# Optimization experiments

Hardware: AMD Instinct MI355X
Metric: run time of the kernel (lower is better)

Reference implementation:

```python
import jax, jax.numpy as jnp
import numpy as np

D = 1024   # embed_dim
L = 8      # num_blocks
H = 8      # num_heads
T = 2048   # temporal length
DH = D // H


def _ln(x, g, b, eps):
    m = jnp.mean(x, axis=-1, keepdims=True)
    v = jnp.var(x, axis=-1, keepdims=True)
    return (x - m) * jax.lax.rsqrt(v + eps) * g + b


def setup_inputs() -> dict:
    key = jax.random.key(0)
    ks = iter(jax.random.split(key, 48))
    s = 0.02
    rn = lambda shape: jax.random.normal(next(ks), shape, jnp.float32) * s
    return {
        "video_features": jax.random.normal(next(ks), (1, T, 1024), jnp.float32),
        "audio_features": jax.random.normal(next(ks), (1, T, 128), jnp.float32),
        "ap_W1": rn((128, D // 2)), "ap_b1": jnp.zeros((D // 2,)),
        "ap_W2": rn((D // 2, D)), "ap_b2": jnp.zeros((D,)),
        "vp_W1": rn((1024, D // 2)), "vp_b1": jnp.zeros((D // 2,)),
        "vp_W2": rn((D // 2, D)), "vp_b2": jnp.zeros((D,)),
        "pre_ln_g": jnp.ones((D,)), "pre_ln_b": jnp.zeros((D,)),
        "blk_Wq": rn((L, D, D)), "blk_bq": jnp.zeros((L, D)),
        "blk_Wk": rn((L, D, D)), "blk_bk": jnp.zeros((L, D)),
        "blk_Wv": rn((L, D, D)), "blk_bv": jnp.zeros((L, D)),
        "blk_Wo": rn((L, D, D)), "blk_bo": jnp.zeros((L, D)),
        "blk_bias_k": rn((L, D)), "blk_bias_v": rn((L, D)),
        "blk_ln1_g": jnp.ones((L, D)), "blk_ln1_b": jnp.zeros((L, D)),
        "blk_ln2_g": jnp.ones((L, D)), "blk_ln2_b": jnp.zeros((L, D)),
        "blk_mW1": rn((L, D, 4 * D)), "blk_mb1": jnp.zeros((L, 4 * D)),
        "blk_mW2": rn((L, 4 * D, D)), "blk_mb2": jnp.zeros((L, D)),
        "lh_W1": rn((D, D // 2)), "lh_b1": jnp.zeros((D // 2,)),
        "lh_W2": rn((D // 2, 1)), "lh_b2": jnp.zeros((1,)),
        "threshold": jnp.float32(0.5),
    }


def reference(video_features, audio_features,
              ap_W1, ap_b1, ap_W2, ap_b2,
              vp_W1, vp_b1, vp_W2, vp_b2,
              pre_ln_g, pre_ln_b,
              blk_Wq, blk_bq, blk_Wk, blk_bk, blk_Wv, blk_bv, blk_Wo, blk_bo,
              blk_bias_k, blk_bias_v,
              blk_ln1_g, blk_ln1_b, blk_ln2_g, blk_ln2_b,
              blk_mW1, blk_mb1, blk_mW2, blk_mb2,
              lh_W1, lh_b1, lh_W2, lh_b2, threshold):
    # projectors (Linear -> ReLU -> Linear)
    a = jax.nn.relu(audio_features @ ap_W1 + ap_b1) @ ap_W2 + ap_b2   # [1,T,D]
    v = jax.nn.relu(video_features @ vp_W1 + vp_b1) @ vp_W2 + vp_b2   # [1,T,D]

    x = _ln(a, pre_ln_g, pre_ln_b, 1e-6)  # pre_transformer_layer LayerNorm

    def block(x, p):
        Wq, bq, Wk, bk, Wv, bv, Wo, bo, bkx, bvx, g1, b1, g2, b2, mW1, mb1, mW2, mb2 = p
        h = _ln(x, g1, b1, 1e-5)
        q = (h @ Wq + bq).reshape(1, T, H, DH)
        # cross K/V from projected video, plus the learned bias_k/bias_v token (add_bias_kv)
        k = jnp.concatenate([v @ Wk + bk, bkx[None, None, :]], axis=1).reshape(1, T + 1, H, DH)
        val = jnp.concatenate([v @ Wv + bv, bvx[None, None, :]], axis=1).reshape(1, T + 1, H, DH)
        scores = jnp.einsum('bthd,bshd->bhts', q, k) * (DH ** -0.5)   # [1,H,T,T+1]
        attn = jax.nn.softmax(scores, axis=-1)
        o = jnp.einsum('bhts,bshd->bthd', attn, val).reshape(1, T, D)
        x = x + o @ Wo + bo
        h2 = _ln(x, g2, b2, 1e-5)
        x = x + jax.nn.gelu(h2 @ mW1 + mb1) @ mW2 + mb2
        return x, None

    ps = (blk_Wq, blk_bq, blk_Wk, blk_bk, blk_Wv, blk_bv, blk_Wo, blk_bo,
          blk_bias_k, blk_bias_v, blk_ln1_g, blk_ln1_b, blk_ln2_g, blk_ln2_b,
          blk_mW1, blk_mb1, blk_mW2, blk_mb2)
    x, _ = jax.lax.scan(block, x, ps)

    # locate head: Linear -> ReLU -> Linear -> Sigmoid
    located = jax.nn.sigmoid(jax.nn.relu(x @ lh_W1 + lh_b1) @ lh_W2 + lh_b2)[..., 0]  # [1,T]

    # on-device run-length segmentation (replaces the per-step python loop)
    clips = (located[0] > threshold).astype(jnp.int32)                 # [T]
    seg_ids = jnp.concatenate([jnp.zeros((1,), jnp.int32),
                               jnp.cumsum((clips[1:] != clips[:-1]).astype(jnp.int32))])
    counts = jax.ops.segment_sum(jnp.ones((T,), jnp.float32), seg_ids, num_segments=T)
    denom = jnp.maximum(counts, 1.0)[:, None]
    # variable-length segment mean pooling (AdaptiveAvgPool1d(1) per segment), padded to T segments
    vid_pool = jax.ops.segment_sum(v[0], seg_ids, num_segments=T) / denom   # [T,D]
    aud_pool = jax.ops.segment_sum(a[0], seg_ids, num_segments=T) / denom   # [T,D]
    seg_types = jax.ops.segment_max(clips, seg_ids, num_segments=T)
    num_seg = seg_ids[-1] + 1
    return vid_pool[None], aud_pool[None], located, seg_ids, seg_types, num_seg
```

## Files before the change

### kernel.cpp

```cpp
#include <hip/hip_runtime.h>
#include <math.h>

typedef float4 f4;
typedef __attribute__((ext_vector_type(8))) short bf8v;
typedef __attribute__((ext_vector_type(4))) float f4v;

#define T_SEQ 2048
#define D_MOD 1024

__device__ __forceinline__ float gelu_f(float x){
    float u = 0.7978845608028654f*(x + 0.044715f*x*x*x);
    return 0.5f*x*(1.0f + tanhf(u));
}

__device__ __forceinline__ unsigned f32_to_pair(float x){
    unsigned u = __float_as_uint(x);
    unsigned hi = (u + 0x7FFFu + ((u >> 16) & 1u)) >> 16;
    float hif = __uint_as_float(hi << 16);
    float lof = x - hif;
    unsigned v = __float_as_uint(lof);
    unsigned lo = (v + 0x7FFFu + ((v >> 16) & 1u)) >> 16;
    return hi | (lo << 16);
}

__device__ __forceinline__ void split2(float x, short& hi, short& lo){
    unsigned u = __float_as_uint(x);
    hi = (short)(u >> 16);
    float rem = x - __uint_as_float(u & 0xFFFF0000u);
    lo = (short)(__float_as_uint(rem) >> 16);
}

__global__ __launch_bounds__(256) void convert1(
    const float* __restrict__ s, unsigned* __restrict__ d, int n4)
{
    const int i = blockIdx.x*256 + threadIdx.x;
    if (i < n4){
        f4 v = ((const f4*)s)[i];
        uint4 o;
        o.x = f32_to_pair(v.x); o.y = f32_to_pair(v.y);
        o.z = f32_to_pair(v.z); o.w = f32_to_pair(v.w);
        ((uint4*)d)[i] = o;
    }
}

__global__ __launch_bounds__(256) void convert6(
    const float* __restrict__ s0, const float* __restrict__ s1,
    const float* __restrict__ s2, const float* __restrict__ s3,
    const float* __restrict__ s4, const float* __restrict__ s5,
    unsigned* __restrict__ d0, unsigned* __restrict__ d1,
    unsigned* __restrict__ d2, unsigned* __restrict__ d3,
    unsigned* __restrict__ d4, unsigned* __restrict__ d5)
{
    const int stride = gridDim.x * 256;
    for (int idx = blockIdx.x*256 + threadIdx.x; idx < 3145728; idx += stride){
        const float* s; unsigned* d; int off;
        if (idx < 1048576){
            const int r = idx >> 18; off = idx & 262143;
            s = (r==0)?s0:(r==1)?s1:(r==2)?s2:s3;
            d = (r==0)?d0:(r==1)?d1:(r==2)?d2:d3;
        } else if (idx < 2097152){ s = s4; d = d4; off = idx - 1048576; }
        else                     { s = s5; d = d5; off = idx - 2097152; }
        f4 v = ((const f4*)s)[off];
        uint4 o;
        o.x = f32_to_pair(v.x); o.y = f32_to_pair(v.y);
        o.z = f32_to_pair(v.z); o.w = f32_to_pair(v.w);
        ((uint4*)d)[off] = o;
    }
}

__global__ __launch_bounds__(256) void gemm_mfma(
    const unsigned* __restrict__ Apr, const unsigned* __restrict__ Wpr,
    const float* __restrict__ bias, const float* __restrict__ res,
    float* __restrict__ Cf, unsigned* __restrict__ Cp,
    int M, int N, int K, int act, int hasres, int outpair)
{
    __shared__ short Ah[2][4][64][8];
    __shared__ short Al[2][4][64][8];
    __shared__ short Bh[2][8][64][8];
    __shared__ short Bl[2][8][64][8];
    const int tid = threadIdx.x;
    const int w = tid >> 6, l = tid & 63;
    const int row0 = blockIdx.y * 64, col0 = blockIdx.x * 128;
    const int mb = (w >> 1) * 2;
    const int nb = (w & 1) * 4;

    f4v acc[2][4];
    #pragma unroll
    for (int i=0;i<2;i++)
        #pragma unroll
        for (int j=0;j<4;j++) acc[i][j] = (f4v){0.f,0.f,0.f,0.f};

    const int b_c4 = (tid & 31) * 4;
    const int b_kg = tid >> 5;

    for (int k0 = 0; k0 < K; k0 += 64){
        if (k0) __syncthreads();
        #pragma unroll
        for (int i=0;i<2;i++){
            const int u = tid + i*256;
            const int ar = u >> 3, kg = u & 7;
            const unsigned* src = Apr + (size_t)(row0 + ar)*K + k0 + kg*8;
            const uint4 p0 = *(const uint4*)src;
            const uint4 p1 = *(const uint4*)(src + 4);
            bf8v hv, lv;
            hv[0]=(short)(p0.x); lv[0]=(short)(p0.x>>16);
            hv[1]=(short)(p0.y); lv[1]=(short)(p0.y>>16);
            hv[2]=(short)(p0.z); lv[2]=(short)(p0.z>>16);
            hv[3]=(short)(p0.w); lv[3]=(short)(p0.w>>16);
            hv[4]=(short)(p1.x); lv[4]=(short)(p1.x>>16);
            hv[5]=(short)(p1.y); lv[5]=(short)(p1.y>>16);
            hv[6]=(short)(p1.z); lv[6]=(short)(p1.z>>16);
            hv[7]=(short)(p1.w); lv[7]=(short)(p1.w>>16);
            const int lane = (ar & 15) | ((kg & 3) << 4);
            const int ks = kg >> 2, mf = ar >> 4;
            *(bf8v*)&Ah[ks][mf][lane][0] = hv;
            *(bf8v*)&Al[ks][mf][lane][0] = lv;
        }
        {
            uint4 r[8];
            #pragma unroll
            for (int j=0;j<8;j++)
                r[j] = *(const uint4*)(Wpr + (size_t)(k0 + b_kg*8 + j)*N + col0 + b_c4);
            #pragma unroll
            for (int c=0;c<4;c++){
                bf8v hv, lv;
                #pragma unroll
                for (int j=0;j<8;j++){
                    const unsigned e = ((const unsigned*)&r[j])[c];
                    hv[j] = (short)e; lv[j] = (short)(e >> 16);
                }
                const int col = b_c4 + c;
                const int lane = (col & 15) | ((b_kg & 3) << 4);
                const int ks = b_kg >> 2, nf = col >> 4;
                *(bf8v*)&Bh[ks][nf][lane][0] = hv;
                *(bf8v*)&Bl[ks][nf][lane][0] = lv;
            }
        }
        __syncthreads();
        #pragma unroll
        for (int ks=0; ks<2; ks++){
            const bf8v ah0 = *(const bf8v*)&Ah[ks][mb+0][l][0];
            const bf8v ah1 = *(const bf8v*)&Ah[ks][mb+1][l][0];
            const bf8v al0 = *(const bf8v*)&Al[ks][mb+0][l][0];
            const bf8v al1 = *(const bf8v*)&Al[ks][mb+1][l][0];
            #pragma unroll
            for (int nf=0; nf<4; nf++){
                const bf8v bh = *(const bf8v*)&Bh[ks][nb+nf][l][0];
                const bf8v bl = *(const bf8v*)&Bl[ks][nb+nf][l][0];
                acc[0][nf] = __builtin_amdgcn_mfma_f32_16x16x32_bf16(ah0, bh, acc[0][nf], 0,0,0);
                acc[0][nf] = __builtin_amdgcn_mfma_f32_16x16x32_bf16(ah0, bl, acc[0][nf], 0,0,0);
                acc[0][nf] = __builtin_amdgcn_mfma_f32_16x16x32_bf16(al0, bh, acc[0][nf], 0,0,0);
                acc[1][nf] = __builtin_amdgcn_mfma_f32_16x16x32_bf16(ah1, bh, acc[1][nf], 0,0,0);
                acc[1][nf] = __builtin_amdgcn_mfma_f32_16x16x32_bf16(ah1, bl, acc[1][nf], 0,0,0);
                acc[1][nf] = __builtin_amdgcn_mfma_f32_16x16x32_bf16(al1, bh, acc[1][nf], 0,0,0);
            }
        }
    }

    const int ecol = l & 15, erow = (l >> 4) * 4;
    #pragma unroll
    for (int mf=0; mf<2; mf++){
        #pragma unroll
        for (int nf=0; nf<4; nf++){
            const int col = col0 + (w&1)*64 + nf*16 + ecol;
            const float bv = bias[col];
            #pragma unroll
            for (int j=0; j<4; j++){
                const int row = row0 + (w>>1)*32 + mf*16 + erow + j;
                float v = acc[mf][nf][j] + bv;
                if (act==1) v = fmaxf(v, 0.f);
                else if (act==2) v = gelu_f(v);
                if (hasres) v += res[(size_t)row*N + col];
                if (outpair) Cp[(size_t)row*N + col] = f32_to_pair(v);
                else         Cf[(size_t)row*N + col] = v;
            }
        }
    }
}

__global__ __launch_bounds__(512) void gemm128k2(
    const float* __restrict__ A, const float* __restrict__ W,
    const float* __restrict__ bias, const float* __restrict__ res,
    float* __restrict__ C, int M, int N, int K, int act, int hasres)
{
    __shared__ float As[2][32][68];
    __shared__ float Ws[2][32][132];
    const int tid = threadIdx.x;
    const int kh = tid >> 8;
    const int t  = tid & 255;
    const int row0 = blockIdx.y*64, col0 = blockIdx.x*128;
    const int ty = t>>4, tx = t&15;
    const int am = t>>2, ak = (t&3)*8;
    const int wk = t>>3, u  = t&7;
    const int K2 = K >> 1;
    const float* Ap = A + (size_t)(row0+am)*K + kh*K2 + ak;
    const float* Wp = W + (size_t)(kh*K2 + wk)*N + col0 + u*16;
    float* Wrow = &Ws[kh][wk][0];

    f4 a0,a1,w0,w1,w2,w3;
    a0 = *(const f4*)(Ap);
    a1 = *(const f4*)(Ap + 4);
    w0 = *(const f4*)(Wp);
    w1 = *(const f4*)(Wp + 4);
    w2 = *(const f4*)(Wp + 8);
    w3 = *(const f4*)(Wp + 12);
    As[kh][ak+0][am]=a0.x; As[kh][ak+1][am]=a0.y; As[kh][ak+2][am]=a0.z; As[kh][ak+3][am]=a0.w;
    As[kh][ak+4][am]=a1.x; As[kh][ak+5][am]=a1.y; As[kh][ak+6][am]=a1.z; As[kh][ak+7][am]=a1.w;
    *(f4*)(Wrow + 8*u)      = w0;
    *(f4*)(Wrow + 8*u + 4)  = w2;
    *(f4*)(Wrow + 64 + 8*u)     = w1;
    *(f4*)(Wrow + 64 + 8*u + 4) = w3;
    __syncthreads();

    float acc[4][8];
    #pragma unroll
    for (int i=0;i<4;i++){
        #pragma unroll
        for (int j=0;j<8;j++) acc[i][j]=0.f;
    }

    int k0 = 0;
    while (true){
        const int kn = k0 + 32;
        const bool more = kn < K2;
        if (more){
            a0 = *(const f4*)(Ap + kn);
            a1 = *(const f4*)(Ap + kn + 4);
            w0 = *(const f4*)(Wp + (size_t)kn*N);
            w1 = *(const f4*)(Wp + (size_t)kn*N + 4);
            w2 = *(const f4*)(Wp + (size_t)kn*N + 8);
            w3 = *(const f4*)(Wp + (size_t)kn*N + 12);
        }
        #pragma unroll
        for (int kk=0;kk<32;kk++){
            f4 a  = *(const f4*)&As[kh][kk][ty*4];
            f4 wA = *(const f4*)&Ws[kh][kk][tx*4];
            f4 wB = *(const f4*)&Ws[kh][kk][64 + tx*4];
            float ar[4] = {a.x,a.y,a.z,a.w};
            #pragma unroll
            for (int i=0;i<4;i++){
                acc[i][0] += ar[i]*wA.x;
                acc[i][1] += ar[i]*wA.y;
                acc[i][2] += ar[i]*wA.z;
                acc[i][3] += ar[i]*wA.w;
                acc[i][4] += ar[i]*wB.x;
                acc[i][5] += ar[i]*wB.y;
                acc[i][6] += ar[i]*wB.z;
                acc[i][7] += ar[i]*wB.w;
            }
        }
        __syncthreads();
        if (!more) break;
        As[kh][ak+0][am]=a0.x; As[kh][ak+1][am]=a0.y; As[kh][ak+2][am]=a0.z; As[kh][ak+3][am]=a0.w;
        As[kh][ak+4][am]=a1.x; As[kh][ak+5][am]=a1.y; As[kh][ak+6][am]=a1.z; As[kh][ak+7][am]=a1.w;
        *(f4*)(Wrow + 8*u)      = w0;
        *(f4*)(Wrow + 8*u + 4)  = w2;
        *(f4*)(Wrow + 64 + 8*u)     = w1;
        *(f4*)(Wrow + 64 + 8*u + 4) = w3;
        __syncthreads();
        k0 = kn;
    }

    float* cs = &Ws[0][0][0];
    if (kh == 1){
        #pragma unroll
        for (int i=0;i<4;i++){
            #pragma unroll
            for (int b=0;b<2;b++){
                f4 p;
                p.x=acc[i][b*4+0]; p.y=acc[i][b*4+1]; p.z=acc[i][b*4+2]; p.w=acc[i][b*4+3];
                *(f4*)(cs + 4*(((i<<1)|b)*256 + t)) = p;
            }
        }
    }
    __syncthreads();
    if (kh == 0){
        #pragma unroll
        for (int i=0;i<4;i++){
            #pragma unroll
            for (int b=0;b<2;b++){
                const f4 p = *(const f4*)(cs + 4*(((i<<1)|b)*256 + t));
                acc[i][b*4+0]+=p.x; acc[i][b*4+1]+=p.y; acc[i][b*4+2]+=p.z; acc[i][b*4+3]+=p.w;
            }
        }
        #pragma unroll
        for (int i=0;i<4;i++){
            const int r = row0 + ty*4 + i;
            #pragma unroll
            for (int half=0; half<2; ++half){
                const int cb = col0 + tx*8 + half*4;
                f4 bv = *(const f4*)(bias + cb);
                float t0 = acc[i][half*4+0] + bv.x;
                float t1 = acc[i][half*4+1] + bv.y;
                float t2 = acc[i][half*4+2] + bv.z;
                float t3 = acc[i][half*4+3] + bv.w;
                if (act==1){ t0=fmaxf(t0,0.f); t1=fmaxf(t1,0.f); t2=fmaxf(t2,0.f); t3=fmaxf(t3,0.f); }
                else if (act==2){ t0=gelu_f(t0); t1=gelu_f(t1); t2=gelu_f(t2); t3=gelu_f(t3); }
                if (hasres){
                    f4 rv = *(const f4*)(res + (size_t)r*N + cb);
                    t0+=rv.x; t1+=rv.y; t2+=rv.z; t3+=rv.w;
                }
                f4 o; o.x=t0; o.y=t1; o.z=t2; o.w=t3;
                *(f4*)(C + (size_t)r*N + cb) = o;
            }
        }
    }
}

__global__ __launch_bounds__(256) void lnrow(
    const float* __restrict__ X, const float* __restrict__ g,
    const float* __restrict__ b, float* __restrict__ out, float eps)
{
    __shared__ float red[4];
    const int row = blockIdx.x, tid = threadIdx.x;
    const float* xp = X + (size_t)row*D_MOD;
    f4 xv = *(const f4*)(xp + tid*4);
    float s = xv.x+xv.y+xv.z+xv.w;
    #pragma unroll
    for (int m=1;m<64;m<<=1) s += __shfl_xor(s, m);
    const int wid = tid>>6, lane = tid&63;
    if (lane==0) red[wid]=s;
    __syncthreads();
    float mean = (red[0]+red[1]+red[2]+red[3]) * (1.0f/1024.0f);
    __syncthreads();
    float d0=xv.x-mean, d1=xv.y-mean, d2=xv.z-mean, d3=xv.w-mean;
    float q = d0*d0+d1*d1+d2*d2+d3*d3;
    #pragma unroll
    for (int m=1;m<64;m<<=1) q += __shfl_xor(q, m);
    if (lane==0) red[wid]=q;
    __syncthreads();
// ... 384 lines not shown
    #pragma unroll
    for (int off=1; off<64; off<<=1){
        int u = __shfl_up(v, off, 64);
        if (lane>=off) v += u;
    }
    if (lane==63) wsum[wid] = v;
    __syncthreads();
    if (tid < 16){
        int w = wsum[tid];
        #pragma unroll
        for (int off=1; off<16; off<<=1){
            int u = __shfl_up(w, off, 16);
            if (tid>=off) w += u;
        }
        wsum[tid] = w;
    }
    __syncthreads();
    int base = (wid>0 ? wsum[wid-1] : 0) + (v - e1);
    segid[t0] = base + e0;
    segid[t1] = base + e1;
    __syncthreads();
    const int ns = segid[2047] + 1;
    for (int t=tid; t<2048; t+=1024){
        if (t==0 || segid[t]!=segid[t-1]) sstart[segid[t]] = t;
    }
    if (tid==0) sstart[ns] = 2048;
    __syncthreads();
    for (int t=tid; t<2048; t+=1024) out_segid[t] = (float)segid[t];
    for (int s=tid; s<2048; s+=1024)
        out_segtype[s] = (s<ns) ? (float)clips[sstart[s]] : -2147483648.0f;
    if (tid==0){ out_numseg[0] = (float)ns; wsi[0] = ns; }
    for (int s=tid; s<=2048; s+=1024) wsi[2+s] = (s<=ns) ? sstart[s] : 0;
}

__global__ __launch_bounds__(256) void segpool(
    const float* __restrict__ V, const float* __restrict__ A,
    const int* __restrict__ wsi, float* __restrict__ out_vid,
    float* __restrict__ out_aud)
{
    const int s = blockIdx.x;
    const int c = threadIdx.x*4;
    const int ns = wsi[0];
    f4 vv; vv.x=0.f; vv.y=0.f; vv.z=0.f; vv.w=0.f;
    f4 av = vv;
    if (s < ns){
        const int st = wsi[2+s], en = wsi[2+s+1];
        for (int r=st; r<en; ++r){
            f4 x = *(const f4*)(V + (size_t)r*D_MOD + c);
            vv.x+=x.x; vv.y+=x.y; vv.z+=x.z; vv.w+=x.w;
            f4 y = *(const f4*)(A + (size_t)r*D_MOD + c);
            av.x+=y.x; av.y+=y.y; av.z+=y.z; av.w+=y.w;
        }
        const float inv = 1.0f/(float)(en-st);
        vv.x*=inv; vv.y*=inv; vv.z*=inv; vv.w*=inv;
        av.x*=inv; av.y*=inv; av.z*=inv; av.w*=inv;
    }
    *(f4*)(out_vid + (size_t)s*D_MOD + c) = vv;
    *(f4*)(out_aud + (size_t)s*D_MOD + c) = av;
}

extern "C" void kernel_launch(void* const* d_in, const int* in_sizes, int n_in,
                              void* d_out, int out_size, void* d_ws, size_t ws_size,
                              hipStream_t stream) {
    (void)in_sizes; (void)n_in; (void)out_size; (void)ws_size;
    const float* video = (const float*)d_in[0];
    const float* audio = (const float*)d_in[1];
    const float* apW1  = (const float*)d_in[2];
    const float* apb1  = (const float*)d_in[3];
    const float* apW2  = (const float*)d_in[4];
    const float* apb2  = (const float*)d_in[5];
    const float* vpW1  = (const float*)d_in[6];
    const float* vpb1  = (const float*)d_in[7];
    const float* vpW2  = (const float*)d_in[8];
    const float* vpb2  = (const float*)d_in[9];
    const float* preg  = (const float*)d_in[10];
    const float* preb  = (const float*)d_in[11];
    const float* bWq   = (const float*)d_in[12];
    const float* bbq   = (const float*)d_in[13];
    const float* bWk   = (const float*)d_in[14];
    const float* bbk   = (const float*)d_in[15];
    const float* bWv   = (const float*)d_in[16];
    const float* bbv   = (const float*)d_in[17];
    const float* bWo   = (const float*)d_in[18];
    const float* bbo   = (const float*)d_in[19];
    const float* bbiask= (const float*)d_in[20];
    const float* bbiasv= (const float*)d_in[21];
    const float* bg1   = (const float*)d_in[22];
    const float* bb1   = (const float*)d_in[23];
    const float* bg2   = (const float*)d_in[24];
    const float* bb2   = (const float*)d_in[25];
    const float* bmW1  = (const float*)d_in[26];
    const float* bmb1  = (const float*)d_in[27];
    const float* bmW2  = (const float*)d_in[28];
    const float* bmb2  = (const float*)d_in[29];
    const float* lhW1  = (const float*)d_in[30];
    const float* lhb1  = (const float*)d_in[31];
    const float* lhW2  = (const float*)d_in[32];
    const float* lhb2  = (const float*)d_in[33];
    const float* thrp  = (const float*)d_in[34];

    float* ws = (float*)d_ws;
    float* V    = ws + 0;
    float* Abuf = ws + 2097152;
    float* X    = ws + 4194304;
    float* H    = ws + 6291456;
    float* Q    = ws + 8388608;
    float* Kb   = ws + 10485760;
    float* Vb   = ws + 12582912;
    float* Obuf = ws + 14680064;
    unsigned* M4p = (unsigned*)(ws + 8388608);
    float* M512 = ws + 16777216;
    float* LOC  = ws + 17825792;
    int*   WSI  = (int*)(ws + 17827840);
    float* ML0  = ws + 17829952;
    float* ML1  = ws + 17862720;
    unsigned* Vp  = (unsigned*)(ws + 17895488);
    unsigned* OPp = (unsigned*)(ws + 19992640);
    unsigned* WQp = (unsigned*)(ws + 22089792);
    unsigned* WKp = (unsigned*)(ws + 23138368);
    unsigned* WVp = (unsigned*)(ws + 24186944);
    unsigned* WOp = (unsigned*)(ws + 25235520);
    unsigned* W1p = (unsigned*)(ws + 26284096);
    unsigned* W2p = (unsigned*)(ws + 30478400);
    unsigned* Hp  = (unsigned*)H;

    float* out = (float*)d_out;
    float* out_vid     = out + 0;
    float* out_aud     = out + 2097152;
    float* out_loc     = out + 4194304;
    float* out_segid   = out + 4196352;
    float* out_segtype = out + 4198400;
    float* out_numseg  = out + 4200448;

    const dim3 B512(512);
    const dim3 B256(256);
    #define GRID128(M,N) dim3((N)/128,(M)/64)
    #define GRIDM(M,N)   dim3((N)/128,(M)/64)

    gemm128k2<<<GRID128(2048,512), B512, 0, stream>>>(audio, apW1, apb1, nullptr, M512, 2048,512,128, 1,0);
    gemm128k2<<<GRID128(2048,1024),B512, 0, stream>>>(M512, apW2, apb2, nullptr, Abuf, 2048,1024,512, 0,0);
    gemm128k2<<<GRID128(2048,512), B512, 0, stream>>>(video, vpW1, vpb1, nullptr, M512, 2048,512,1024, 1,0);
    gemm128k2<<<GRID128(2048,1024),B512, 0, stream>>>(M512, vpW2, vpb2, nullptr, V,    2048,1024,512, 0,0);
    lnrow<<<2048, B256, 0, stream>>>(Abuf, preg, preb, X, 1e-6f);
    convert1<<<2048, B256, 0, stream>>>(V, Vp, 524288);

    for (int l=0; l<8; ++l){
        const size_t wo = (size_t)l*1024*1024;
        const size_t bo = (size_t)l*1024;
        const size_t mo1 = (size_t)l*1024*4096;
        convert6<<<1536, B256, 0, stream>>>(bWq+wo, bWk+wo, bWv+wo, bWo+wo,
                                            bmW1+mo1, bmW2+mo1,
                                            WQp, WKp, WVp, WOp, W1p, W2p);
        lnrow_pair<<<2048, B256, 0, stream>>>(X, bg1+bo, bb1+bo, Hp, 1e-5f);
        gemm_mfma<<<GRIDM(2048,1024), B256, 0, stream>>>(Hp, WQp, bbq+bo, nullptr, Q,  nullptr, 2048,1024,1024, 0,0,0);
        gemm_mfma<<<GRIDM(2048,1024), B256, 0, stream>>>(Vp, WKp, bbk+bo, nullptr, Kb, nullptr, 2048,1024,1024, 0,0,0);
        gemm_mfma<<<GRIDM(2048,1024), B256, 0, stream>>>(Vp, WVp, bbv+bo, nullptr, Vb, nullptr, 2048,1024,1024, 0,0,0);
        attn_mfma<<<256, B256, 0, stream>>>(Q, Kb, Vb, Obuf, H, ML0, ML1);
        attn_combine<<<2048, B256, 0, stream>>>(Q, bbiask+bo, bbiasv+bo, Obuf, H, ML0, ML1, OPp);
        gemm_mfma<<<GRIDM(2048,1024), B256, 0, stream>>>(OPp, WOp, bbo+bo, X, X, nullptr, 2048,1024,1024, 0,1,0);
        lnrow_pair<<<2048, B256, 0, stream>>>(X, bg2+bo, bb2+bo, Hp, 1e-5f);
        gemm_mfma<<<GRIDM(2048,4096), B256, 0, stream>>>(Hp, W1p, bmb1+(size_t)l*4096, nullptr, nullptr, M4p, 2048,4096,1024, 2,0,1);
        gemm_mfma<<<GRIDM(2048,1024), B256, 0, stream>>>(M4p, W2p, bmb2+bo, X, X, nullptr, 2048,1024,4096, 0,1,0);
    }

    gemm128k2<<<GRID128(2048,512), B512, 0, stream>>>(X, lhW1, lhb1, nullptr, M512, 2048,512,1024, 1,0);
    locate_head<<<2048, dim3(64), 0, stream>>>(M512, lhW2, lhb2, LOC, out_loc);
    segscan<<<1, dim3(1024), 0, stream>>>(LOC, thrp, out_segid, out_segtype, out_numseg, WSI);
    segpool<<<2048, B256, 0, stream>>>(V, Abuf, WSI, out_vid, out_aud);
}
```

Before: 4.710 ms.

## Add split-K MFMA GEMM with 512 threads for N=1024 projections

```diff
diff --git a/kernel.cpp b/kernel.cpp
--- a/kernel.cpp
+++ b/kernel.cpp
@@ -176,6 +176,167 @@
             }
         }
     }
+}
+
+__global__ __launch_bounds__(512) void gemm_mfma2(
+    const unsigned* __restrict__ Apr, const unsigned* __restrict__ Wpr,
+    const float* __restrict__ bias, const float* __restrict__ res,
+    float* __restrict__ Cf, unsigned* __restrict__ Cp,
+    int M, int N, int K, int act, int hasres, int outpair)
+{
+    __shared__ short Ah[2][2][4][64][8];
+    __shared__ short Al[2][2][4][64][8];
+    __shared__ short Bh[2][2][8][64][8];
+    __shared__ short Bl[2][2][8][64][8];
+    const int tid = threadIdx.x;
+    const int kh = tid >> 8;
+    const int t  = tid & 255;
+    const int w = t >> 6, l = t & 63;
+    const int row0 = blockIdx.y * 64, col0 = blockIdx.x * 128;
+    const int mb = (w >> 1) * 2;
+    const int nb = (w & 1) * 4;
+    const int K2 = K >> 1;
+    const int kbase = kh * K2;
+    const int b_c4 = (t & 31) * 4;
+    const int b_kg = t >> 5;
+    const int a_r0 = t >> 3,      a_kg0 = t & 7;
+    const int a_r1 = (t+256) >> 3, a_kg1 = (t+256) & 7;
+
+    f4v acc[2][4];
+    #pragma unroll
+    for (int i=0;i<2;i++)
+        #pragma unroll
+        for (int j=0;j<4;j++) acc[i][j] = (f4v){0.f,0.f,0.f,0.f};
+
+    uint4 pa0[2], pa1[2], pb[8];
+
+    {
+        const unsigned* s0 = Apr + (size_t)(row0 + a_r0)*K + kbase + a_kg0*8;
+        const unsigned* s1 = Apr + (size_t)(row0 + a_r1)*K + kbase + a_kg1*8;
+        pa0[0] = *(const uint4*)s0; pa0[1] = *(const uint4*)(s0+4);
+        pa1[0] = *(const uint4*)s1; pa1[1] = *(const uint4*)(s1+4);
+        #pragma unroll
+        for (int j=0;j<8;j++)
+            pb[j] = *(const uint4*)(Wpr + (size_t)(kbase + b_kg*8 + j)*N + col0 + b_c4);
+    }
+
+    #define STAGE_A(pr, ar, kg) { \
+        bf8v hv, lv; \
+        hv[0]=(short)(pr[0].x); lv[0]=(short)(pr[0].x>>16); \
+        hv[1]=(short)(pr[0].y); lv[1]=(short)(pr[0].y>>16); \
+        hv[2]=(short)(pr[0].z); lv[2]=(short)(pr[0].z>>16); \
+        hv[3]=(short)(pr[0].w); lv[3]=(short)(pr[0].w>>16); \
+        hv[4]=(short)(pr[1].x); lv[4]=(short)(pr[1].x>>16); \
+        hv[5]=(short)(pr[1].y); lv[5]=(short)(pr[1].y>>16); \
+        hv[6]=(short)(pr[1].z); lv[6]=(short)(pr[1].z>>16); \
+        hv[7]=(short)(pr[1].w); lv[7]=(short)(pr[1].w>>16); \
+        const int lane_ = ((ar) & 15) | (((kg) & 3) << 4); \
+        *(bf8v*)&Ah[kh][(kg)>>2][(ar)>>4][lane_][0] = hv; \
+        *(bf8v*)&Al[kh][(kg)>>2][(ar)>>4][lane_][0] = lv; }
+
+    #define STAGE_B() { \
+        _Pragma("unroll") \
+        for (int c=0;c<4;c++){ \
+            bf8v hv, lv; \
+            _Pragma("unroll") \
+            for (int j=0;j<8;j++){ \
+                const unsigned e = ((const unsigned*)&pb[j])[c]; \
+                hv[j] = (short)e; lv[j] = (short)(e >> 16); \
+            } \
+            const int col_ = b_c4 + c; \
+            const int lane_ = (col_ & 15) | ((b_kg & 3) << 4); \
+            *(bf8v*)&Bh[kh][b_kg>>2][col_>>4][lane_][0] = hv; \
+            *(bf8v*)&Bl[kh][b_kg>>2][col_>>4][lane_][0] = lv; } }
+
+    STAGE_A(pa0, a_r0, a_kg0)
+    STAGE_A(pa1, a_r1, a_kg1)
+    STAGE_B()
+    __syncthreads();
+
+    int k0 = 0;
+    while (true){
+        const int kn = k0 + 64;
+        const bool more = kn < K2;
+        if (more){
+            const unsigned* s0 = Apr + (size_t)(row0 + a_r0)*K + kbase + kn + a_kg0*8;
+            const unsigned* s1 = Apr + (size_t)(row0 + a_r1)*K + kbase + kn + a_kg1*8;
+            pa0[0] = *(const uint4*)s0; pa0[1] = *(const uint4*)(s0+4);
+            pa1[0] = *(const uint4*)s1; pa1[1] = *(const uint4*)(s1+4);
+            #pragma unroll
+            for (int j=0;j<8;j++)
+                pb[j] = *(const uint4*)(Wpr + (size_t)(kbase + kn + b_kg*8 + j)*N + col0 + b_c4);
+        }
+        #pragma unroll
+        for (int ks=0; ks<2; ks++){
+            const bf8v ah0 = *(const bf8v*)&Ah[kh][ks][mb+0][l][0];
+            const bf8v ah1 = *(const bf8v*)&Ah[kh][ks][mb+1][l][0];
+            const bf8v al0 = *(const bf8v*)&Al[kh][ks][mb+0][l][0];
+            const bf8v al1 = *(const bf8v*)&Al[kh][ks][mb+1][l][0];
+            #pragma unroll
+            for (int nf=0; nf<4; nf++){
+                const bf8v bh = *(const bf8v*)&Bh[kh][ks][nb+nf][l][0];
+                const bf8v bl = *(const bf8v*)&Bl[kh][ks][nb+nf][l][0];
+                acc[0][nf] = __builtin_amdgcn_mfma_f32_16x16x32_bf16(ah0, bh, acc[0][nf], 0,0,0);
+                acc[0][nf] = __builtin_amdgcn_mfma_f32_16x16x32_bf16(ah0, bl, acc[0][nf], 0,0,0);
+                acc[0][nf] = __builtin_amdgcn_mfma_f32_16x16x32_bf16(al0, bh, acc[0][nf], 0,0,0);
+                acc[1][nf] = __builtin_amdgcn_mfma_f32_16x16x32_bf16(ah1, bh, acc[1][nf], 0,0,0);
+                acc[1][nf] = __builtin_amdgcn_mfma_f32_16x16x32_bf16(ah1, bl, acc[1][nf], 0,0,0);
+                acc[1][nf] = __builtin_amdgcn_mfma_f32_16x16x32_bf16(al1, bh, acc[1][nf], 0,0,0);
+            }
+        }
+        __syncthreads();
+        if (!more) break;
+        STAGE_A(pa0, a_r0, a_kg0)
+        STAGE_A(pa1, a_r1, a_kg1)
+        STAGE_B()
+        __syncthreads();
+        k0 = kn;
+    }
+
+    float* cs = (float*)&Ah[0][0][0][0][0];
+    if (kh == 1){
+        #pragma unroll
+        for (int mf=0; mf<2; mf++)
+            #pragma unroll
+            for (int nf=0; nf<4; nf++){
+                f4 p;
+                p.x=acc[mf][nf][0]; p.y=acc[mf][nf][1];
+                p.z=acc[mf][nf][2]; p.w=acc[mf][nf][3];
+                *(f4*)(cs + 4*(((mf*4+nf))*256 + t)) = p;
+            }
+    }
+    __syncthreads();
+    if (kh == 0){
+        #pragma unroll
+        for (int mf=0; mf<2; mf++)
+            #pragma unroll
+            for (int nf=0; nf<4; nf++){
+                const f4 p = *(const f4*)(cs + 4*(((mf*4+nf))*256 + t));
+                acc[mf][nf][0]+=p.x; acc[mf][nf][1]+=p.y;
+                acc[mf][nf][2]+=p.z; acc[mf][nf][3]+=p.w;
+            }
+        const int ecol = l & 15, erow = (l >> 4) * 4;
+        #pragma unroll
+        for (int mf=0; mf<2; mf++){
+            #pragma unroll
+            for (int nf=0; nf<4; nf++){
+                const int col = col0 + (w&1)*64 + nf*16 + ecol;
+                const float bv = bias[col];
+                #pragma unroll
+                for (int j=0; j<4; j++){
+                    const int row = row0 + (w>>1)*32 + mf*16 + erow + j;
+                    float v = acc[mf][nf][j] + bv;
+                    if (act==1) v = fmaxf(v, 0.f);
+                    else if (act==2) v = gelu_f(v);
+                    if (hasres) v += res[(size_t)row*N + col];
+                    if (outpair) Cp[(size_t)row*N + col] = f32_to_pair(v);
+                    else         Cf[(size_t)row*N + col] = v;
+                }
+            }
+        }
+    }
+    #undef STAGE_A
+    #undef STAGE_B
 }
 
 __global__ __launch_bounds__(512) void gemm128k2(
@@ -866,15 +1027,15 @@
                                             bmW1+mo1, bmW2+mo1,
                                             WQp, WKp, WVp, WOp, W1p, W2p);
         lnrow_pair<<<2048, B256, 0, stream>>>(X, bg1+bo, bb1+bo, Hp, 1e-5f);
-        gemm_mfma<<<GRIDM(2048,1024), B256, 0, stream>>>(Hp, WQp, bbq+bo, nullptr, Q,  nullptr, 2048,1024,1024, 0,0,0);
-        gemm_mfma<<<GRIDM(2048,1024), B256, 0, stream>>>(Vp, WKp, bbk+bo, nullptr, Kb, nullptr, 2048,1024,1024, 0,0,0);
-        gemm_mfma<<<GRIDM(2048,1024), B256, 0, stream>>>(Vp, WVp, bbv+bo, nullptr, Vb, nullptr, 2048,1024,1024, 0,0,0);
+        gemm_mfma2<<<GRIDM(2048,1024), B512, 0, stream>>>(Hp, WQp, bbq+bo, nullptr, Q,  nullptr, 2048,1024,1024, 0,0,0);
+        gemm_mfma2<<<GRIDM(2048,1024), B512, 0, stream>>>(Vp, WKp, bbk+bo, nullptr, Kb, nullptr, 2048,1024,1024, 0,0,0);
+        gemm_mfma2<<<GRIDM(2048,1024), B512, 0, stream>>>(Vp, WVp, bbv+bo, nullptr, Vb, nullptr, 2048,1024,1024, 0,0,0);
         attn_mfma<<<256, B256, 0, stream>>>(Q, Kb, Vb, Obuf, H, ML0, ML1);
         attn_combine<<<2048, B256, 0, stream>>>(Q, bbiask+bo, bbiasv+bo, Obuf, H, ML0, ML1, OPp);
-        gemm_mfma<<<GRIDM(2048,1024), B256, 0, stream>>>(OPp, WOp, bbo+bo, X, X, nullptr, 2048,1024,1024, 0,1,0);
+        gemm_mfma2<<<GRIDM(2048,1024), B512, 0, stream>>>(OPp, WOp, bbo+bo, X, X, nullptr, 2048,1024,1024, 0,1,0);
         lnrow_pair<<<2048, B256, 0, stream>>>(X, bg2+bo, bb2+bo, Hp, 1e-5f);
         gemm_mfma<<<GRIDM(2048,4096), B256, 0, stream>>>(Hp, W1p, bmb1+(size_t)l*4096, nullptr, nullptr, M4p, 2048,4096,1024, 2,0,1);
-        gemm_mfma<<<GRIDM(2048,1024), B256, 0, stream>>>(M4p, W2p, bmb2+bo, X, X, nullptr, 2048,1024,4096, 0,1,0);
+        gemm_mfma2<<<GRIDM(2048,1024), B512, 0, stream>>>(M4p, W2p, bmb2+bo, X, X, nullptr, 2048,1024,4096, 0,1,0);
     }
 
     gemm128k2<<<GRID128(2048,512), B512, 0, stream>>>(X, lhW1, lhb1, nullptr, M512, 2048,512,1024, 1,0);
```

Result: faster. 4.272 ms (-9.3%).

## Split-K across two wave groups with register-prefetched double buffering in MFMA GEMM

Applied to the files above, without the earlier changes.

```diff
diff --git a/kernel.cpp b/kernel.cpp
--- a/kernel.cpp
+++ b/kernel.cpp
@@ -68,21 +68,31 @@
     }
 }
 
-__global__ __launch_bounds__(256) void gemm_mfma(
+__global__ __launch_bounds__(512) __attribute__((amdgpu_waves_per_eu(2,2)))
+void gemm_mfma2(
     const unsigned* __restrict__ Apr, const unsigned* __restrict__ Wpr,
     const float* __restrict__ bias, const float* __restrict__ res,
     float* __restrict__ Cf, unsigned* __restrict__ Cp,
     int M, int N, int K, int act, int hasres, int outpair)
 {
-    __shared__ short Ah[2][4][64][8];
-    __shared__ short Al[2][4][64][8];
-    __shared__ short Bh[2][8][64][8];
-    __shared__ short Bl[2][8][64][8];
+    __shared__ short Ah[2][2][4][64][8];
+    __shared__ short Al[2][2][4][64][8];
+    __shared__ short Bh[2][2][8][64][8];
+    __shared__ short Bl[2][2][8][64][8];
     const int tid = threadIdx.x;
-    const int w = tid >> 6, l = tid & 63;
+    const int kh = tid >> 8;
+    const int t  = tid & 255;
+    const int w = t >> 6, l = t & 63;
     const int row0 = blockIdx.y * 64, col0 = blockIdx.x * 128;
     const int mb = (w >> 1) * 2;
     const int nb = (w & 1) * 4;
+    const int K2 = K >> 1;
+    const int kbase = kh * K2;
+    const int NT = K2 >> 6;
+    const int b_c4 = (t & 31) * 4;
+    const int b_kg = t >> 5;
+    const int a_r0 = t >> 3,       a_kg0 = t & 7;
+    const int a_r1 = (t+256) >> 3, a_kg1 = (t+256) & 7;
 
     f4v acc[2][4];
     #pragma unroll
@@ -90,92 +100,134 @@
         #pragma unroll
         for (int j=0;j<4;j++) acc[i][j] = (f4v){0.f,0.f,0.f,0.f};
 
-    const int b_c4 = (tid & 31) * 4;
-    const int b_kg = tid >> 5;
-
-    for (int k0 = 0; k0 < K; k0 += 64){
-        if (k0) __syncthreads();
-        #pragma unroll
-        for (int i=0;i<2;i++){
-            const int u = tid + i*256;
-            const int ar = u >> 3, kg = u & 7;
-            const unsigned* src = Apr + (size_t)(row0 + ar)*K + k0 + kg*8;
-            const uint4 p0 = *(const uint4*)src;
-            const uint4 p1 = *(const uint4*)(src + 4);
-            bf8v hv, lv;
-            hv[0]=(short)(p0.x); lv[0]=(short)(p0.x>>16);
-            hv[1]=(short)(p0.y); lv[1]=(short)(p0.y>>16);
-            hv[2]=(short)(p0.z); lv[2]=(short)(p0.z>>16);
-            hv[3]=(short)(p0.w); lv[3]=(short)(p0.w>>16);
-            hv[4]=(short)(p1.x); lv[4]=(short)(p1.x>>16);
-            hv[5]=(short)(p1.y); lv[5]=(short)(p1.y>>16);
-            hv[6]=(short)(p1.z); lv[6]=(short)(p1.z>>16);
-            hv[7]=(short)(p1.w); lv[7]=(short)(p1.w>>16);
-            const int lane = (ar & 15) | ((kg & 3) << 4);
-            const int ks = kg >> 2, mf = ar >> 4;
-            *(bf8v*)&Ah[ks][mf][lane][0] = hv;
-            *(bf8v*)&Al[ks][mf][lane][0] = lv;
-        }
-        {
-            uint4 r[8];
-            #pragma unroll
-            for (int j=0;j<8;j++)
-                r[j] = *(const uint4*)(Wpr + (size_t)(k0 + b_kg*8 + j)*N + col0 + b_c4);
-            #pragma unroll
-            for (int c=0;c<4;c++){
-                bf8v hv, lv;
+    uint4 eA0[2], eA1[2], eB[8];
+    uint4 oA0[2], oA1[2], oB[8];
+
+    #define LOADT(A0v,A1v,Bv,kt) { \
+        const int kk_ = kbase + (kt)*64; \
+        const unsigned* s0_ = Apr + (size_t)(row0 + a_r0)*K + kk_ + a_kg0*8; \
+        const unsigned* s1_ = Apr + (size_t)(row0 + a_r1)*K + kk_ + a_kg1*8; \
+        A0v[0] = *(const uint4*)s0_; A0v[1] = *(const uint4*)(s0_+4); \
+        A1v[0] = *(const uint4*)s1_; A1v[1] = *(const uint4*)(s1_+4); \
+        _Pragma("unroll") \
+        for (int j_=0;j_<8;j_++) \
+            Bv[j_] = *(const uint4*)(Wpr + (size_t)(kk_ + b_kg*8 + j_)*N + col0 + b_c4); }
+
+    #define STAGE_A(pr, ar, kg) { \
+        bf8v hv, lv; \
+        hv[0]=(short)(pr[0].x); lv[0]=(short)(pr[0].x>>16); \
+        hv[1]=(short)(pr[0].y); lv[1]=(short)(pr[0].y>>16); \
+        hv[2]=(short)(pr[0].z); lv[2]=(short)(pr[0].z>>16); \
+        hv[3]=(short)(pr[0].w); lv[3]=(short)(pr[0].w>>16); \
+        hv[4]=(short)(pr[1].x); lv[4]=(short)(pr[1].x>>16); \
+        hv[5]=(short)(pr[1].y); lv[5]=(short)(pr[1].y>>16); \
+        hv[6]=(short)(pr[1].z); lv[6]=(short)(pr[1].z>>16); \
+        hv[7]=(short)(pr[1].w); lv[7]=(short)(pr[1].w>>16); \
+        const int lane_ = ((ar) & 15) | (((kg) & 3) << 4); \
+        *(bf8v*)&Ah[kh][(kg)>>2][(ar)>>4][lane_][0] = hv; \
+        *(bf8v*)&Al[kh][(kg)>>2][(ar)>>4][lane_][0] = lv; }
+
+    #define STAGE_B(Bv) { \
+        _Pragma("unroll") \
+        for (int c_=0;c_<4;c_++){ \
+            bf8v hv, lv; \
+            _Pragma("unroll") \
+            for (int j_=0;j_<8;j_++){ \
+                const unsigned e_ = ((const unsigned*)&Bv[j_])[c_]; \
+                hv[j_] = (short)e_; lv[j_] = (short)(e_ >> 16); \
+            } \
+            const int col_ = b_c4 + c_; \
+            const int lane_ = (col_ & 15) | ((b_kg & 3) << 4); \
+            *(bf8v*)&Bh[kh][b_kg>>2][col_>>4][lane_][0] = hv; \
+            *(bf8v*)&Bl[kh][b_kg>>2][col_>>4][lane_][0] = lv; } }
+
+    #define STAGE(A0v,A1v,Bv) { STAGE_A(A0v, a_r0, a_kg0) STAGE_A(A1v, a_r1, a_kg1) STAGE_B(Bv) }
+
+    #define COMPUTE() { \
+        _Pragma("unroll") \
+        for (int ks=0; ks<2; ks++){ \
+            const bf8v ah0 = *(const bf8v*)&Ah[kh][ks][mb+0][l][0]; \
+            const bf8v ah1 = *(const bf8v*)&Ah[kh][ks][mb+1][l][0]; \
+            const bf8v al0 = *(const bf8v*)&Al[kh][ks][mb+0][l][0]; \
+            const bf8v al1 = *(const bf8v*)&Al[kh][ks][mb+1][l][0]; \
+            _Pragma("unroll") \
+            for (int nf=0; nf<4; nf++){ \
+                const bf8v bh = *(const bf8v*)&Bh[kh][ks][nb+nf][l][0]; \
+                const bf8v bl = *(const bf8v*)&Bl[kh][ks][nb+nf][l][0]; \
+                acc[0][nf] = __builtin_amdgcn_mfma_f32_16x16x32_bf16(ah0, bh, acc[0][nf], 0,0,0); \
+                acc[0][nf] = __builtin_amdgcn_mfma_f32_16x16x32_bf16(ah0, bl, acc[0][nf], 0,0,0); \
+                acc[0][nf] = __builtin_amdgcn_mfma_f32_16x16x32_bf16(al0, bh, acc[0][nf], 0,0,0); \
+                acc[1][nf] = __builtin_amdgcn_mfma_f32_16x16x32_bf16(ah1, bh, acc[1][nf], 0,0,0); \
+                acc[1][nf] = __builtin_amdgcn_mfma_f32_16x16x32_bf16(ah1, bl, acc[1][nf], 0,0,0); \
+                acc[1][nf] = __builtin_amdgcn_mfma_f32_16x16x32_bf16(al1, bh, acc[1][nf], 0,0,0); \
+            } \
+        } }
+
+    LOADT(eA0,eA1,eB, 0)
+    LOADT(oA0,oA1,oB, 1)
+    STAGE(eA0,eA1,eB)
+    __syncthreads();
+
+    for (int kt=0; kt<NT; kt+=2){
+        COMPUTE();
+        if (kt+2 < NT) LOADT(eA0,eA1,eB, kt+2)
+        __syncthreads();
+        STAGE(oA0,oA1,oB)
+        __syncthreads();
+        COMPUTE();
+        if (kt+3 < NT) LOADT(oA0,oA1,oB, kt+3)
+        __syncthreads();
+        if (kt+2 < NT) { STAGE(eA0,eA1,eB) }
+        __syncthreads();
+    }
+
+    float* cs = (float*)&Ah[0][0][0][0][0];
+    if (kh == 1){
+        #pragma unroll
+        for (int mf=0; mf<2; mf++)
+            #pragma unroll
+            for (int nf=0; nf<4; nf++){
+                f4 p;
+                p.x=acc[mf][nf][0]; p.y=acc[mf][nf][1];
+                p.z=acc[mf][nf][2]; p.w=acc[mf][nf][3];
+                *(f4*)(cs + 4*(((mf*4+nf))*256 + t)) = p;
+            }
+    }
+    __syncthreads();
+    if (kh == 0){
+        #pragma unroll
+        for (int mf=0; mf<2; mf++)
+            #pragma unroll
+            for (int nf=0; nf<4; nf++){
+                const f4 p = *(const f4*)(cs + 4*(((mf*4+nf))*256 + t));
+                acc[mf][nf][0]+=p.x; acc[mf][nf][1]+=p.y;
+                acc[mf][nf][2]+=p.z; acc[mf][nf][3]+=p.w;
+            }
+        const int ecol = l & 15, erow = (l >> 4) * 4;
+        #pragma unroll
+        for (int mf=0; mf<2; mf++){
+            #pragma unroll
+            for (int nf=0; nf<4; nf++){
+                const int col = col0 + (w&1)*64 + nf*16 + ecol;
+                const float bv = bias[col];
                 #pragma unroll
-                for (int j=0;j<8;j++){
-                    const unsigned e = ((const unsigned*)&r[j])[c];
-                    hv[j] = (short)e; lv[j] = (short)(e >> 16);
+                for (int j=0; j<4; j++){
+                    const int row = row0 + (w>>1)*32 + mf*16 + erow + j;
+                    float v = acc[mf][nf][j] + bv;
+                    if (act==1) v = fmaxf(v, 0.f);
+                    else if (act==2) v = gelu_f(v);
+                    if (hasres) v += res[(size_t)row*N + col];
+                    if (outpair) Cp[(size_t)row*N + col] = f32_to_pair(v);
+                    else         Cf[(size_t)row*N + col] = v;
                 }
-                const int col = b_c4 + c;
-                const int lane = (col & 15) | ((b_kg & 3) << 4);
-                const int ks = b_kg >> 2, nf = col >> 4;
-                *(bf8v*)&Bh[ks][nf][lane][0] = hv;
-                *(bf8v*)&Bl[ks][nf][lane][0] = lv;
-            }
-        }
-        __syncthreads();
-        #pragma unroll
-        for (int ks=0; ks<2; ks++){
-            const bf8v ah0 = *(const bf8v*)&Ah[ks][mb+0][l][0];
-            const bf8v ah1 = *(const bf8v*)&Ah[ks][mb+1][l][0];
-            const bf8v al0 = *(const bf8v*)&Al[ks][mb+0][l][0];
-            const bf8v al1 = *(const bf8v*)&Al[ks][mb+1][l][0];
-            #pragma unroll
-            for (int nf=0; nf<4; nf++){
-                const bf8v bh = *(const bf8v*)&Bh[ks][nb+nf][l][0];
-                const bf8v bl = *(const bf8v*)&Bl[ks][nb+nf][l][0];
-                acc[0][nf] = __builtin_amdgcn_mfma_f32_16x16x32_bf16(ah0, bh, acc[0][nf], 0,0,0);
-                acc[0][nf] = __builtin_amdgcn_mfma_f32_16x16x32_bf16(ah0, bl, acc[0][nf], 0,0,0);
-                acc[0][nf] = __builtin_amdgcn_mfma_f32_16x16x32_bf16(al0, bh, acc[0][nf], 0,0,0);
-                acc[1][nf] = __builtin_amdgcn_mfma_f32_16x16x32_bf16(ah1, bh, acc[1][nf], 0,0,0);
-                acc[1][nf] = __builtin_amdgcn_mfma_f32_16x16x32_bf16(ah1, bl, acc[1][nf], 0,0,0);
-                acc[1][nf] = __builtin_amdgcn_mfma_f32_16x16x32_bf16(al1, bh, acc[1][nf], 0,0,0);
-            }
-        }
-    }
-
-    const int ecol = l & 15, erow = (l >> 4) * 4;
-    #pragma unroll
-    for (int mf=0; mf<2; mf++){
-        #pragma unroll
-        for (int nf=0; nf<4; nf++){
-            const int col = col0 + (w&1)*64 + nf*16 + ecol;
-            const float bv = bias[col];
-            #pragma unroll
-            for (int j=0; j<4; j++){
-                const int row = row0 + (w>>1)*32 + mf*16 + erow + j;
-                float v = acc[mf][nf][j] + bv;
-                if (act==1) v = fmaxf(v, 0.f);
-                else if (act==2) v = gelu_f(v);
-                if (hasres) v += res[(size_t)row*N + col];
-                if (outpair) Cp[(size_t)row*N + col] = f32_to_pair(v);
-                else         Cf[(size_t)row*N + col] = v;
-            }
-        }
-    }
+            }
+        }
+    }
+    #undef LOADT
+    #undef STAGE_A
+    #undef STAGE_B
+    #undef STAGE
+    #undef COMPUTE
 }
 
 __global__ __launch_bounds__(512) void gemm128k2(
@@ -866,15 +918,15 @@
                                             bmW1+mo1, bmW2+mo1,
                                             WQp, WKp, WVp, WOp, W1p, W2p);
         lnrow_pair<<<2048, B256, 0, stream>>>(X, bg1+bo, bb1+bo, Hp, 1e-5f);
-        gemm_mfma<<<GRIDM(2048,1024), B256, 0, stream>>>(Hp, WQp, bbq+bo, nullptr, Q,  nullptr, 2048,1024,1024, 0,0,0);
-        gemm_mfma<<<GRIDM(2048,1024), B256, 0, stream>>>(Vp, WKp, bbk+bo, nullptr, Kb, nullptr, 2048,1024,1024, 0,0,0);
-        gemm_mfma<<<GRIDM(2048,1024), B256, 0, stream>>>(Vp, WVp, bbv+bo, nullptr, Vb, nullptr, 2048,1024,1024, 0,0,0);
+        gemm_mfma2<<<GRIDM(2048,1024), B512, 0, stream>>>(Hp, WQp, bbq+bo, nullptr, Q,  nullptr, 2048,1024,1024, 0,0,0);
+        gemm_mfma2<<<GRIDM(2048,1024), B512, 0, stream>>>(Vp, WKp, bbk+bo, nullptr, Kb, nullptr, 2048,1024,1024, 0,0,0);
+        gemm_mfma2<<<GRIDM(2048,1024), B512, 0, stream>>>(Vp, WVp, bbv+bo, nullptr, Vb, nullptr, 2048,1024,1024, 0,0,0);
         attn_mfma<<<256, B256, 0, stream>>>(Q, Kb, Vb, Obuf, H, ML0, ML1);
         attn_combine<<<2048, B256, 0, stream>>>(Q, bbiask+bo, bbiasv+bo, Obuf, H, ML0, ML1, OPp);
-        gemm_mfma<<<GRIDM(2048,1024), B256, 0, stream>>>(OPp, WOp, bbo+bo, X, X, nullptr, 2048,1024,1024, 0,1,0);
+        gemm_mfma2<<<GRIDM(2048,1024), B512, 0, stream>>>(OPp, WOp, bbo+bo, X, X, nullptr, 2048,1024,1024, 0,1,0);
         lnrow_pair<<<2048, B256, 0, stream>>>(X, bg2+bo, bb2+bo, Hp, 1e-5f);
-        gemm_mfma<<<GRIDM(2048,4096), B256, 0, stream>>>(Hp, W1p, bmb1+(size_t)l*4096, nullptr, nullptr, M4p, 2048,4096,1024, 2,0,1);
-        gemm_mfma<<<GRIDM(2048,1024), B256, 0, stream>>>(M4p, W2p, bmb2+bo, X, X, nullptr, 2048,1024,4096, 0,1,0);
+        gemm_mfma2<<<GRIDM(2048,4096), B512, 0, stream>>>(Hp, W1p, bmb1+(size_t)l*4096, nullptr, nullptr, M4p, 2048,4096,1024, 2,0,1);
+        gemm_mfma2<<<GRIDM(2048,1024), B512, 0, stream>>>(M4p, W2p, bmb2+bo, X, X, nullptr, 2048,1024,4096, 0,1,0);
     }
 
     gemm128k2<<<GRID128(2048,512), B512, 0, stream>>>(X, lhW1, lhb1, nullptr, M512, 2048,512,1024, 1,0);
```

Result: faster. 4.438 ms (-5.8%).
